# Kernel optimization log

Measured on AMD Instinct MI355X. Metric: run time of the kernel, lower is better.

The kernel has to match this reference:

```python
import jax, jax.numpy as jnp
import numpy as np

N = 50000   # nodes
E = 800000  # directed edges (built as reverse pairs so rev mapping is exact)
F = 64      # node_feat_dim
FE = 64     # edge_feat_dim
M = 64      # message_dim
S = 3       # num_status
L = 4       # number_layers

def _lin(key, din, dout):
    w = jax.random.normal(key, (din, dout), jnp.float32) * np.float32(1.0 / np.sqrt(din))
    return w, jnp.zeros((dout,), jnp.float32)

def setup_inputs() -> dict:
    key = jax.random.key(0)
    ks = jax.random.split(key, 16)
    half = E // 2
    s = jax.random.randint(ks[0], (half,), 0, N)
    t = jax.random.randint(ks[1], (half,), 0, N)
    src = jnp.concatenate([s, t])                      # source node of each edge
    tgt = jnp.concatenate([t, s])                      # target node of each edge
    rev = jnp.concatenate([jnp.arange(half, E), jnp.arange(half)])  # reverse-edge index
    inp = dict(src=src, tgt=tgt, rev=rev)
    inp['edge_feat_raw'] = jax.random.uniform(ks[2], (E, 1), jnp.float32)
    inp['node_prob'] = jax.random.uniform(ks[3], (N, 1), jnp.float32)
    inp['node_seed'] = (jax.random.uniform(ks[4], (N, 1)) < 0.05).astype(jnp.float32)
    inp['W_node'], inp['b_node'] = _lin(ks[5], 2, F)
    inp['W_edge'], inp['b_edge'] = _lin(ks[6], 1, FE)
    inp['W_init'], inp['b_init'] = _lin(ks[7], F + FE, M)
    inp['W_aggr'], inp['b_aggr'] = _lin(ks[8], M, M)
    inp['W_out'], inp['b_out'] = _lin(ks[9], M + F, S)
    inp['W_me'], inp['b_me'] = _lin(ks[10], FE + M, M)
    inp['W_mp'], inp['b_mp'] = _lin(ks[11], M, M)
    inp['W_ih'] = jax.random.normal(ks[12], (3 * M, M), jnp.float32) * np.float32(1.0 / np.sqrt(M))
    inp['W_hh'] = jax.random.normal(ks[13], (3 * M, M), jnp.float32) * np.float32(1.0 / np.sqrt(M))
    inp['b_ih'] = jnp.zeros((3 * M,), jnp.float32)
    inp['b_hh'] = jnp.zeros((3 * M,), jnp.float32)
    return inp

def reference(src, tgt, rev, edge_feat_raw, node_prob, node_seed,
              W_node, b_node, W_edge, b_edge, W_init, b_init,
              W_aggr, b_aggr, W_out, b_out, W_me, b_me, W_mp, b_mp,
              W_ih, W_hh, b_ih, b_hh):
    relu = jax.nn.relu
    node_feat = relu(jnp.concatenate([node_prob, node_seed], 1) @ W_node + b_node)  # [N,F]
    snode_feat = node_feat[src]                                                      # snode2edge gather [E,F]
    edge_feat = relu(edge_feat_raw @ W_edge + b_edge)                                # [E,FE]
    message = relu(jnp.concatenate([snode_feat, edge_feat], 1) @ W_init + b_init)    # [E,M]

    def nodes_out(msg):
        agg = jax.ops.segment_sum(msg, tgt, num_segments=N)                          # edge2tnode scatter-add
        agg = relu(agg @ W_aggr + b_aggr)
        logits = relu(jnp.concatenate([agg, node_feat], 1) @ W_out + b_out)
        return jax.nn.log_softmax(logits, axis=1)                                    # [N,S]

    def gru(x, h):  # torch.nn.GRUCell semantics
        gi = x @ W_ih.T + b_ih
        gh = h @ W_hh.T + b_hh
        ir, iz, in_ = jnp.split(gi, 3, axis=1)
        hr, hz, hn = jnp.split(gh, 3, axis=1)
        r = jax.nn.sigmoid(ir + hr)
        z = jax.nn.sigmoid(iz + hz)
        n = jnp.tanh(in_ + r * hn)
        return (1.0 - z) * n + z * h

    marg = [nodes_out(message)]
    deltas = []
    for _ in range(L):
        m = relu(jnp.concatenate([message, edge_feat], 1) @ W_me + b_me)
        node_agg = jax.ops.segment_sum(m, tgt, num_segments=N)
        m = node_agg[src] - m[rev]                                                   # nb_matrix (non-backtracking) spmm
        m = relu(m @ W_mp + b_mp)
        message = gru(m, message)
        marg.append(nodes_out(message))
        deltas.append(jnp.max(jnp.abs(jnp.exp(marg[-2][:, -1]) - jnp.exp(marg[-1][:, -1]))))
    return jnp.stack(marg, 0), jnp.stack(deltas)
```

## Files before the change

### kernel.cpp

```cpp
#include <hip/hip_runtime.h>
#include <hip/hip_fp16.h>

typedef _Float16 half8 __attribute__((ext_vector_type(8)));
typedef float floatx4 __attribute__((ext_vector_type(4)));

#define DEV static __device__ __forceinline__

DEV float sigmoidf_(float x) { return 1.f / (1.f + __expf(-x)); }
DEV float tanh_fast(float x) {
    x = fminf(fmaxf(x, -15.f), 15.f);
    float e2 = __expf(2.f * x);
    return (e2 - 1.f) / (e2 + 1.f);
}
DEV unsigned short f2h_(float f) {
    __half h = __float2half_rn(f);
    return *reinterpret_cast<unsigned short*>(&h);
}
DEV float h2f_(unsigned short u) {
    __half h = *reinterpret_cast<__half*>(&u);
    return __half2float(h);
}
DEV float loadElem(const float* p) { return *p; }
DEV float loadElem(const unsigned short* p) { return h2f_(*p); }
DEV void storeMsg(float* p, float v) { *p = v; }
DEV void storeMsg(unsigned short* p, float v) { *p = f2h_(v); }

DEV half8 afrag(const float* __restrict__ p, int koff) {
    float4 a = *reinterpret_cast<const float4*>(p + koff);
    float4 b = *reinterpret_cast<const float4*>(p + koff + 4);
    half8 h;
    h[0] = (_Float16)a.x; h[1] = (_Float16)a.y; h[2] = (_Float16)a.z; h[3] = (_Float16)a.w;
    h[4] = (_Float16)b.x; h[5] = (_Float16)b.y; h[6] = (_Float16)b.z; h[7] = (_Float16)b.w;
    return h;
}
DEV half8 afrag(const unsigned short* __restrict__ p, int koff) {
    uint4 v = *reinterpret_cast<const uint4*>(p + koff);
    return __builtin_bit_cast(half8, v);
}
DEV half8 h8load(const _Float16* __restrict__ p) {
    return *reinterpret_cast<const half8*>(p);
}
DEV half8 effrag(float er, const float* __restrict__ We,
                 const float* __restrict__ be, int k0) {
    float4 w0 = *reinterpret_cast<const float4*>(We + k0);
    float4 w1 = *reinterpret_cast<const float4*>(We + k0 + 4);
    float4 b0 = *reinterpret_cast<const float4*>(be + k0);
    float4 b1 = *reinterpret_cast<const float4*>(be + k0 + 4);
    half8 h;
    h[0] = (_Float16)fmaxf(fmaf(er, w0.x, b0.x), 0.f);
    h[1] = (_Float16)fmaxf(fmaf(er, w0.y, b0.y), 0.f);
    h[2] = (_Float16)fmaxf(fmaf(er, w0.z, b0.z), 0.f);
    h[3] = (_Float16)fmaxf(fmaf(er, w0.w, b0.w), 0.f);
    h[4] = (_Float16)fmaxf(fmaf(er, w1.x, b1.x), 0.f);
    h[5] = (_Float16)fmaxf(fmaf(er, w1.y, b1.y), 0.f);
    h[6] = (_Float16)fmaxf(fmaf(er, w1.z, b1.z), 0.f);
    h[7] = (_Float16)fmaxf(fmaf(er, w1.w, b1.w), 0.f);
    return h;
}
DEV void load8(const float* __restrict__ p, float x[8]) {
    const float4* q = reinterpret_cast<const float4*>(p);
    float4 a = q[0], b = q[1];
    x[0] = a.x; x[1] = a.y; x[2] = a.z; x[3] = a.w;
    x[4] = b.x; x[5] = b.y; x[6] = b.z; x[7] = b.w;
}

__global__ void k_deg(const int* __restrict__ tgt, int* __restrict__ deg, int E) {
    int e = blockIdx.x * blockDim.x + threadIdx.x;
    if (e < E) atomicAdd(&deg[tgt[e]], 1);
}

__global__ __launch_bounds__(1024)
void k_scan(const int* __restrict__ deg, int* __restrict__ row_ptr,
            int* __restrict__ cursor, int N) {
    __shared__ int part[1024];
    int tid = threadIdx.x;
    int chunk = (N + 1023) / 1024;
    int lo = tid * chunk, hi = min(lo + chunk, N);
    int s = 0;
    for (int i = lo; i < hi; i++) s += deg[i];
    part[tid] = s;
    __syncthreads();
    for (int off = 1; off < 1024; off <<= 1) {
        int v = (tid >= off) ? part[tid - off] : 0;
        __syncthreads();
        part[tid] += v;
        __syncthreads();
    }
    int base = (tid == 0) ? 0 : part[tid - 1];
    for (int i = lo; i < hi; i++) {
        row_ptr[i] = base;
        cursor[i] = base;
        base += deg[i];
    }
    if (tid == 1023) row_ptr[N] = part[1023];
}

__global__ void k_fill(const int* __restrict__ tgt, int* __restrict__ cursor,
                       int* __restrict__ col_idx, int E) {
    int e = blockIdx.x * blockDim.x + threadIdx.x;
    if (e < E) {
        int pos = atomicAdd(&cursor[tgt[e]], 1);
        col_idx[pos] = e;
    }
}

__global__ void k_prep(const float* __restrict__ Wme, const float* __restrict__ Wmp,
                       const float* __restrict__ Wi, const float* __restrict__ Wih,
                       const float* __restrict__ Whh, _Float16* __restrict__ wp) {
    int t = blockIdx.x * blockDim.x + threadIdx.x;
    if (t < 8192) { int n = t >> 7, k = t & 127; wp[t] = (_Float16)Wme[k * 64 + n]; return; }
    int u = t - 8192;
    if (u < 4096) { int n = u >> 6, k = u & 63; wp[8192 + u] = (_Float16)Wmp[k * 64 + n]; return; }
    u -= 4096;
    if (u < 4096) { int n = u >> 6, k = u & 63; wp[12288 + u] = (_Float16)Wi[(64 + k) * 64 + n]; return; }
    u -= 4096;
    if (u < 12288) { wp[16384 + u] = (_Float16)Wih[u]; return; }
    u -= 12288;
    if (u < 12288) { wp[28672 + u] = (_Float16)Whh[u]; return; }
}

__global__ __launch_bounds__(256)
void k_zn(const float* __restrict__ prob, const float* __restrict__ seedp,
          const float* __restrict__ Wn, const float* __restrict__ bn,
          const float* __restrict__ Wi, const float* __restrict__ bi,
          float* __restrict__ zn, int N) {
    int n = blockIdx.x * blockDim.x + threadIdx.x;
    if (n >= N) return;
    float p = prob[n], sd = seedp[n];
    float acc[64];
#pragma unroll
    for (int j = 0; j < 64; j++) acc[j] = bi[j];
#pragma unroll 1
    for (int k = 0; k < 64; k++) {
        float nf = fmaxf(fmaf(p, Wn[k], fmaf(sd, Wn[64 + k], bn[k])), 0.f);
        const float* w = Wi + k * 64;
#pragma unroll
        for (int j = 0; j < 64; j++) acc[j] = fmaf(nf, w[j], acc[j]);
    }
    float4* q = reinterpret_cast<float4*>(zn + (size_t)n * 64);
#pragma unroll
    for (int c = 0; c < 16; c++)
        q[c] = make_float4(acc[4 * c], acc[4 * c + 1], acc[4 * c + 2], acc[4 * c + 3]);
}

template <typename MsgT>
__global__ __launch_bounds__(256)
void k_init_mfma(const int* __restrict__ src, const float* __restrict__ eraw,
                 const float* __restrict__ We, const float* __restrict__ be,
                 const _Float16* __restrict__ WibT, const float* __restrict__ zn,
                 MsgT* __restrict__ message, int E) {
    int wid = (blockIdx.x * blockDim.x + threadIdx.x) >> 6;
    int rowbase = wid * 64;
    if (rowbase >= E) return;
    int lane = threadIdx.x & 63, q = lane >> 4, m16 = lane & 15, kq8 = q * 8;
    floatx4 zero4 = {0.f, 0.f, 0.f, 0.f};
    floatx4 acc[4][4];
#pragma unroll
    for (int a = 0; a < 4; a++)
#pragma unroll
        for (int b = 0; b < 4; b++) acc[a][b] = zero4;
#pragma unroll
    for (int ks = 0; ks < 2; ks++) {
        int k0 = ks * 32 + kq8;
        half8 B[4];
#pragma unroll
        for (int nt = 0; nt < 4; nt++) B[nt] = h8load(WibT + (nt * 16 + m16) * 64 + k0);
#pragma unroll
        for (int rt = 0; rt < 4; rt++) {
            int row = min(rowbase + rt * 16 + m16, E - 1);
            half8 A = effrag(eraw[row], We, be, k0);
#pragma unroll
            for (int nt = 0; nt < 4; nt++)
                acc[rt][nt] = __builtin_amdgcn_mfma_f32_16x16x32_f16(A, B[nt], acc[rt][nt], 0, 0, 0);
        }
    }
#pragma unroll
    for (int nt = 0; nt < 4; nt++) {
        int col = nt * 16 + m16;
#pragma unroll
        for (int rt = 0; rt < 4; rt++)
#pragma unroll
            for (int r = 0; r < 4; r++) {
                int row = rowbase + rt * 16 + q * 4 + r;
                if (row < E) {
                    int s = src[row];
                    float v = acc[rt][nt][r] + zn[(size_t)s * 64 + col];
                    storeMsg(message + (size_t)row * 64 + col, fmaxf(v, 0.f));
                }
            }
    }
}

template <typename MsgT>
__global__ __launch_bounds__(256)
void k_edge_m_mfma(const float* __restrict__ eraw, const float* __restrict__ We,
                   const float* __restrict__ be, const _Float16* __restrict__ WmeT,
                   const float* __restrict__ bme, const MsgT* __restrict__ message,
                   unsigned short* __restrict__ m_buf, int E) {
    int wid = (blockIdx.x * blockDim.x + threadIdx.x) >> 6;
    int rowbase = wid * 64;
    if (rowbase >= E) return;
    int lane = threadIdx.x & 63, q = lane >> 4, m16 = lane & 15, kq8 = q * 8;
    floatx4 zero4 = {0.f, 0.f, 0.f, 0.f};
    floatx4 acc[4][4];
#pragma unroll
    for (int a = 0; a < 4; a++)
#pragma unroll
        for (int b = 0; b < 4; b++) acc[a][b] = zero4;
#pragma unroll
    for (int ks = 0; ks < 4; ks++) {
        int k0 = ks * 32 + kq8;
        half8 B[4];
#pragma unroll
        for (int nt = 0; nt < 4; nt++) B[nt] = h8load(WmeT + (nt * 16 + m16) * 128 + k0);
#pragma unroll
        for (int rt = 0; rt < 4; rt++) {
            int row = min(rowbase + rt * 16 + m16, E - 1);
            half8 A = (ks < 2) ? afrag(message + (size_t)row * 64, k0)
                               : effrag(eraw[row], We, be, k0 - 64);
#pragma unroll
            for (int nt = 0; nt < 4; nt++)
                acc[rt][nt] = __builtin_amdgcn_mfma_f32_16x16x32_f16(A, B[nt], acc[rt][nt], 0, 0, 0);
        }
    }
#pragma unroll
    for (int nt = 0; nt < 4; nt++) {
        int col = nt * 16 + m16;
        float bb = bme[col];
#pragma unroll
        for (int rt = 0; rt < 4; rt++)
#pragma unroll
            for (int r = 0; r < 4; r++) {
                int row = rowbase + rt * 16 + q * 4 + r;
                if (row < E)
                    m_buf[(size_t)row * 64 + col] = f2h_(fmaxf(acc[rt][nt][r] + bb, 0.f));
            }
    }
}

template <typename MsgT>
__global__ __launch_bounds__(256)
void k_gru_mfma(const int* __restrict__ src, const int* __restrict__ rev,
                const float* __restrict__ node_agg,
                const unsigned short* __restrict__ m_buf,
                const _Float16* __restrict__ WmpT, const float* __restrict__ bmp,
                const _Float16* __restrict__ WihP, const _Float16* __restrict__ WhhP,
                const float* __restrict__ bih, const float* __restrict__ bhh,
                MsgT* __restrict__ message, int E) {
    __shared__ _Float16 uT[4][64 * 72];
    int wid = (blockIdx.x * blockDim.x + threadIdx.x) >> 6;
    int rowbase = wid * 64;
    if (rowbase >= E) return;
    int w = threadIdx.x >> 6;
    int lane = threadIdx.x & 63, q = lane >> 4, m16 = lane & 15, kq8 = q * 8;
    floatx4 zero4 = {0.f, 0.f, 0.f, 0.f};

    floatx4 accU[4][4];
#pragma unroll
    for (int a = 0; a < 4; a++)
#pragma unroll
        for (int b = 0; b < 4; b++) accU[a][b] = zero4;
#pragma unroll
    for (int ks = 0; ks < 2; ks++) {
        int k0 = ks * 32 + kq8;
        half8 B[4];
#pragma unroll
        for (int nt = 0; nt < 4; nt++) B[nt] = h8load(WmpT + (nt * 16 + m16) * 64 + k0);
#pragma unroll
        for (int rt = 0; rt < 4; rt++) {
            int row = min(rowbase + rt * 16 + m16, E - 1);
            int s = src[row], rv = rev[row];
            const float* na = node_agg + (size_t)s * 64 + k0;
            float4 a0 = *reinterpret_cast<const float4*>(na);
            float4 a1 = *reinterpret_cast<const float4*>(na + 4);
            uint4 mv = *reinterpret_cast<const uint4*>(m_buf + (size_t)rv * 64 + k0);
            half8 mh = __builtin_bit_cast(half8, mv);
            half8 A;
            A[0] = (_Float16)(a0.x - (float)mh[0]); A[1] = (_Float16)(a0.y - (float)mh[1]);
            A[2] = (_Float16)(a0.z - (float)mh[2]); A[3] = (_Float16)(a0.w - (float)mh[3]);
            A[4] = (_Float16)(a1.x - (float)mh[4]); A[5] = (_Float16)(a1.y - (float)mh[5]);
            A[6] = (_Float16)(a1.z - (float)mh[6]); A[7] = (_Float16)(a1.w - (float)mh[7]);
#pragma unroll
            for (int nt = 0; nt < 4; nt++)
                accU[rt][nt] = __builtin_amdgcn_mfma_f32_16x16x32_f16(A, B[nt], accU[rt][nt], 0, 0, 0);
        }
    }
#pragma unroll
    for (int nt = 0; nt < 4; nt++) {
        int col = nt * 16 + m16;
        float bb = bmp[col];
#pragma unroll
        for (int rt = 0; rt < 4; rt++)
#pragma unroll
            for (int r = 0; r < 4; r++) {
                int rl = rt * 16 + q * 4 + r;
                uT[w][rl * 72 + col] = (_Float16)fmaxf(accU[rt][nt][r] + bb, 0.f);
            }
    }
    half8 au[4][2], ah[4][2];
#pragma unroll
    for (int rt = 0; rt < 4; rt++)
#pragma unroll
        for (int ks = 0; ks < 2; ks++) {
            au[rt][ks] = *reinterpret_cast<const half8*>(
                &uT[w][(rt * 16 + m16) * 72 + ks * 32 + kq8]);
            int row = min(rowbase + rt * 16 + m16, E - 1);
            ah[rt][ks] = afrag(message + (size_t)row * 64, ks * 32 + kq8);
        }
#pragma unroll 1
    for (int nt = 0; nt < 4; nt++) {
        int col = nt * 16 + m16;
        half8 Bir[2], Biz[2], Bin[2], Bhr[2], Bhz[2], Bhn[2];
#pragma unroll
        for (int ks = 0; ks < 2; ks++) {
            int k0 = ks * 32 + kq8;
            Bir[ks] = h8load(WihP + (size_t)(0 + col) * 64 + k0);
            Biz[ks] = h8load(WihP + (size_t)(64 + col) * 64 + k0);
            Bin[ks] = h8load(WihP + (size_t)(128 + col) * 64 + k0);
            Bhr[ks] = h8load(WhhP + (size_t)(0 + col) * 64 + k0);
            Bhz[ks] = h8load(WhhP + (size_t)(64 + col) * 64 + k0);
            Bhn[ks] = h8load(WhhP + (size_t)(128 + col) * 64 + k0);
        }
        floatx4 ar[4], az[4], ain[4], ahn[4];
#pragma unroll
        for (int rt = 0; rt < 4; rt++) { ar[rt] = zero4; az[rt] = zero4; ain[rt] = zero4; ahn[rt] = zero4; }
#pragma unroll
        for (int ks = 0; ks < 2; ks++)
#pragma unroll
            for (int rt = 0; rt < 4; rt++) {
                ar[rt] = __builtin_amdgcn_mfma_f32_16x16x32_f16(au[rt][ks], Bir[ks], ar[rt], 0, 0, 0);
                ar[rt] = __builtin_amdgcn_mfma_f32_16x16x32_f16(ah[rt][ks], Bhr[ks], ar[rt], 0, 0, 0);
                az[rt] = __builtin_amdgcn_mfma_f32_16x16x32_f16(au[rt][ks], Biz[ks], az[rt], 0, 0, 0);
                az[rt] = __builtin_amdgcn_mfma_f32_16x16x32_f16(ah[rt][ks], Bhz[ks], az[rt], 0, 0, 0);
                ain[rt] = __builtin_amdgcn_mfma_f32_16x16x32_f16(au[rt][ks], Bin[ks], ain[rt], 0, 0, 0);
                ahn[rt] = __builtin_amdgcn_mfma_f32_16x16x32_f16(ah[rt][ks], Bhn[ks], ahn[rt], 0, 0, 0);
            }
        float br_ = bih[col] + bhh[col];
        float bz_ = bih[64 + col] + bhh[64 + col];
        float bin_ = bih[128 + col];
        float bhn_ = bhh[128 + col];
#pragma unroll
        for (int rt = 0; rt < 4; rt++)
#pragma unroll
            for (int r = 0; r < 4; r++) {
                int row = rowbase + rt * 16 + q * 4 + r;
                if (row < E) {
                    float rr = sigmoidf_(ar[rt][r] + br_);
                    float zz = sigmoidf_(az[rt][r] + bz_);
                    float nn = tanh_fast(ain[rt][r] + bin_ + rr * (ahn[rt][r] + bhn_));
                    MsgT* mp = message + (size_t)row * 64 + col;
                    float hv = loadElem(mp);
                    storeMsg(mp, fmaf(zz, hv - nn, nn));
                }
            }
    }
}

template <typename T>
__global__ __launch_bounds__(256)
void k_agg(const int* __restrict__ row_ptr, const int* __restrict__ col_idx,
           const T* __restrict__ rows, float* __restrict__ out, int N) {
    int wid = (blockIdx.x * blockDim.x + threadIdx.x) >> 6;
    int lane = threadIdx.x & 63;
    if (wid >= N) return;
    int beg = row_ptr[wid], end = row_ptr[wid + 1];
    float acc = 0.f;
    int i = beg;
    for (; i + 1 < end; i += 2) {
        int e0 = __builtin_amdgcn_readfirstlane(col_idx[i]);
        int e1 = __builtin_amdgcn_readfirstlane(col_idx[i + 1]);
        acc += loadElem(rows + (size_t)e0 * 64 + lane);
        acc += loadElem(rows + (size_t)e1 * 64 + lane);
    }
    if (i < end) {
        int e0 = __builtin_amdgcn_readfirstlane(col_idx[i]);
        acc += loadElem(rows + (size_t)e0 * 64 + lane);
    }
    out[(size_t)wid * 64 + lane] = acc;
}

__global__ __launch_bounds__(256, 2)
void k_nodes(const float* __restrict__ node_agg, const float* __restrict__ prob,
             const float* __restrict__ seedp,
             const float* __restrict__ Wn, const float* __restrict__ bn,
             const float* __restrict__ Wa, const float* __restrict__ ba,
             const float* __restrict__ Wo, const float* __restrict__ bo,
             float* __restrict__ marg, float* __restrict__ prev_p2,
             float* __restrict__ deltas_f, int layer, int N) {
    int n = blockIdx.x * blockDim.x + threadIdx.x;
    if (n >= N) return;
    float a[64];
#pragma unroll
    for (int j = 0; j < 64; j++) a[j] = ba[j];
    const float* ag = node_agg + (size_t)n * 64;
#pragma unroll 1
    for (int c = 0; c < 8; c++) {
        float v[8];
        load8(ag + 8 * c, v);
#pragma unroll
        for (int i = 0; i < 8; i++) {
            const float* w = Wa + (8 * c + i) * 64;
#pragma unroll
            for (int j = 0; j < 64; j++) a[j] = fmaf(v[i], w[j], a[j]);
        }
    }
    float l0 = bo[0], l1 = bo[1], l2 = bo[2];
#pragma unroll
    for (int k = 0; k < 64; k++) {
        float ak = fmaxf(a[k], 0.f);
        l0 = fmaf(ak, Wo[k * 3 + 0], l0);
        l1 = fmaf(ak, Wo[k * 3 + 1], l1);
        l2 = fmaf(ak, Wo[k * 3 + 2], l2);
    }
    float p = prob[n], sd = seedp[n];
#pragma unroll 1
    for (int k = 0; k < 64; k++) {
        float nf = fmaxf(fmaf(p, Wn[k], fmaf(sd, Wn[64 + k], bn[k])), 0.f);
        l0 = fmaf(nf, Wo[(64 + k) * 3 + 0], l0);
        l1 = fmaf(nf, Wo[(64 + k) * 3 + 1], l1);
        l2 = fmaf(nf, Wo[(64 + k) * 3 + 2], l2);
    }
    l0 = fmaxf(l0, 0.f); l1 = fmaxf(l1, 0.f); l2 = fmaxf(l2, 0.f);
    float mx = fmaxf(l0, fmaxf(l1, l2));
    float ssum = __expf(l0 - mx) + __expf(l1 - mx) + __expf(l2 - mx);
    float lse = mx + logf(ssum);
    float o0 = l0 - lse, o1 = l1 - lse, o2 = l2 - lse;
    float* out = marg + ((size_t)layer * N + n) * 3;
    out[0] = o0; out[1] = o1; out[2] = o2;
    float p2 = __expf(o2);
    if (layer > 0) {
        float d = fabsf(p2 - prev_p2[n]);
        atomicMax(reinterpret_cast<unsigned int*>(deltas_f + (layer - 1)),
                  __float_as_uint(d));
    }
    prev_p2[n] = p2;
}

__global__ void k_deltas_out(const float* __restrict__ deltas_f,
                             float* __restrict__ out, int L) {
    int i = threadIdx.x;
    if (i < L) out[i] = deltas_f[i];
}

template <typename MsgT>
static void run_pipeline(void* const* d_in, int E, int N, MsgT* message,
                         unsigned short* m_buf, float* node_agg, _Float16* wp,
                         int* deg, int* row_ptr, int* cursor, int* col_idx,
                         float* prev_p2, float* deltas_f, float* marg,
                         float* deltas_out, hipStream_t stream) {
    const int* src = (const int*)d_in[0];
    const int* tgt = (const int*)d_in[1];
    const int* rev = (const int*)d_in[2];
    const float* eraw = (const float*)d_in[3];
    const float* prob = (const float*)d_in[4];
    const float* seedp = (const float*)d_in[5];
    const float* Wn = (const float*)d_in[6];  const float* bn = (const float*)d_in[7];
    const float* We = (const float*)d_in[8];  const float* be = (const float*)d_in[9];
    const float* Wi = (const float*)d_in[10]; const float* bi = (const float*)d_in[11];
    const float* Wa = (const float*)d_in[12]; const float* ba = (const float*)d_in[13];
    const float* Wo = (const float*)d_in[14]; const float* bo = (const float*)d_in[15];
    const float* Wme = (const float*)d_in[16]; const float* bme = (const float*)d_in[17];
    const float* Wmp = (const float*)d_in[18]; const float* bmp = (const float*)d_in[19];
    const float* Wih = (const float*)d_in[20]; const float* Whh = (const float*)d_in[21];
    const float* bih = (const float*)d_in[22]; const float* bhh = (const float*)d_in[23];

    const _Float16* WmeT = wp;
    const _Float16* WmpT = wp + 8192;
    const _Float16* WibT = wp + 12288;
    const _Float16* WihP = wp + 16384;
    const _Float16* WhhP = wp + 28672;

    const int L = 4;
    dim3 blk(256);
    dim3 eg((E + 255) / 256), ng((N + 255) / 256);
    dim3 ag((N + 3) / 4);
    int waves = (E + 63) / 64;
    dim3 mg((waves + 3) / 4);

    hipMemsetAsync(deg, 0, (size_t)N * 4, stream);
    hipMemsetAsync(deltas_f, 0, L * sizeof(float), stream);
    k_deg<<<eg, blk, 0, stream>>>(tgt, deg, E);
    k_scan<<<1, 1024, 0, stream>>>(deg, row_ptr, cursor, N);
    k_fill<<<eg, blk, 0, stream>>>(tgt, cursor, col_idx, E);
    k_prep<<<160, 256, 0, stream>>>(Wme, Wmp, Wi, Wih, Whh, wp);
    k_zn<<<ng, blk, 0, stream>>>(prob, seedp, Wn, bn, Wi, bi, node_agg, N);
    k_init_mfma<MsgT><<<mg, blk, 0, stream>>>(src, eraw, We, be, WibT,
                                              node_agg, message, E);
    k_agg<MsgT><<<ag, blk, 0, stream>>>(row_ptr, col_idx, message, node_agg, N);
    k_nodes<<<ng, blk, 0, stream>>>(node_agg, prob, seedp, Wn, bn, Wa, ba, Wo, bo,
                                    marg, prev_p2, deltas_f, 0, N);
    for (int l = 0; l < L; l++) {
        k_edge_m_mfma<MsgT><<<mg, blk, 0, stream>>>(eraw, We, be, WmeT, bme,
                                                    message, m_buf, E);
        k_agg<unsigned short><<<ag, blk, 0, stream>>>(row_ptr, col_idx, m_buf,
                                                      node_agg, N);
        k_gru_mfma<MsgT><<<mg, blk, 0, stream>>>(src, rev, node_agg, m_buf,
                                                 WmpT, bmp, WihP, WhhP, bih, bhh,
                                                 message, E);
        k_agg<MsgT><<<ag, blk, 0, stream>>>(row_ptr, col_idx, message, node_agg, N);
        k_nodes<<<ng, blk, 0, stream>>>(node_agg, prob, seedp, Wn, bn, Wa, ba,
                                        Wo, bo, marg, prev_p2, deltas_f, l + 1, N);
    }
    k_deltas_out<<<1, 64, 0, stream>>>(deltas_f, deltas_out, L);
}

extern "C" void kernel_launch(void* const* d_in, const int* in_sizes, int n_in,
                              void* d_out, int out_size, void* d_ws, size_t ws_size,
                              hipStream_t stream) {
    const int E = in_sizes[0];
    const int N = in_sizes[4];
    const int L = 4, S = 3;

    float* marg = (float*)d_out;
    float* deltas_out = marg + (size_t)(L + 1) * N * S;

    char* ws = (char*)d_ws;
    float* deltas_f = (float*)ws;
    float* prev_p2 = (float*)(ws + 16);
    int* deg = (int*)(prev_p2 + N);
    int* row_ptr = deg + N;
    int* cursor = row_ptr + N + 1;
    int* col_idx = cursor + N;
    char* p = (char*)(col_idx + E);
    p = (char*)(((uintptr_t)p + 255) & ~(uintptr_t)255);
    _Float16* wp = (_Float16*)p;
    p += 40960 * 2;
    p = (char*)(((uintptr_t)p + 255) & ~(uintptr_t)255);
    float* node_agg = (float*)p;
    p += (size_t)N * 64 * 4;
    p = (char*)(((uintptr_t)p + 255) & ~(uintptr_t)255);
    size_t head = (size_t)(p - ws);
    size_t msg_f32 = (size_t)E * 64 * 4;
    size_t msg_f16 = (size_t)E * 64 * 2;
    size_t m_f16 = (size_t)E * 64 * 2;

    if (ws_size >= head + msg_f32 + m_f16) {
        float* message = (float*)p;
        unsigned short* m_buf = (unsigned short*)(p + msg_f32);
        run_pipeline<float>(d_in, E, N, message, m_buf, node_agg, wp,
                            deg, row_ptr, cursor, col_idx,
                            prev_p2, deltas_f, marg, deltas_out, stream);
    } else {
        unsigned short* message = (unsigned short*)p;
        unsigned short* m_buf = (unsigned short*)(p + msg_f16);
        run_pipeline<unsigned short>(d_in, E, N, message, m_buf, node_agg, wp,
                                     deg, row_ptr, cursor, col_idx,
                                     prev_p2, deltas_f, marg, deltas_out, stream);
    }
}
```

Baseline: 2.469 ms.

## Split edge kernels into full/tail launches, use 32-bit indexing, extract h via MFMA

The edge MFMA kernels are templated on a FULL flag. Full 256-row blocks skip row clamping and bounds checks, and a single separate launch handles the tail. Address arithmetic moves from size_t to unsigned 32-bit to save 64-bit integer ops. The GRU kernel recovers the previous hidden value from the already loaded A fragments with an identity-matrix MFMA instead of reloading it from global memory. The CSR aggregation loop is unrolled by four. Together these cut instruction count and memory traffic, at the cost of an extra tail launch and an overflow risk if E*64 exceeds 32 bits.

```diff
diff --git a/kernel.cpp b/kernel.cpp
--- a/kernel.cpp
+++ b/kernel.cpp
@@ -25,16 +25,16 @@
 DEV void storeMsg(float* p, float v) { *p = v; }
 DEV void storeMsg(unsigned short* p, float v) { *p = f2h_(v); }
 
-DEV half8 afrag(const float* __restrict__ p, int koff) {
-    float4 a = *reinterpret_cast<const float4*>(p + koff);
-    float4 b = *reinterpret_cast<const float4*>(p + koff + 4);
+DEV half8 afrag(const float* __restrict__ p, unsigned off) {
+    float4 a = *reinterpret_cast<const float4*>(p + off);
+    float4 b = *reinterpret_cast<const float4*>(p + off + 4);
     half8 h;
     h[0] = (_Float16)a.x; h[1] = (_Float16)a.y; h[2] = (_Float16)a.z; h[3] = (_Float16)a.w;
     h[4] = (_Float16)b.x; h[5] = (_Float16)b.y; h[6] = (_Float16)b.z; h[7] = (_Float16)b.w;
     return h;
 }
-DEV half8 afrag(const unsigned short* __restrict__ p, int koff) {
-    uint4 v = *reinterpret_cast<const uint4*>(p + koff);
+DEV half8 afrag(const unsigned short* __restrict__ p, unsigned off) {
+    uint4 v = *reinterpret_cast<const uint4*>(p + off);
     return __builtin_bit_cast(half8, v);
 }
 DEV half8 h8load(const _Float16* __restrict__ p) {
@@ -143,14 +143,14 @@
         q[c] = make_float4(acc[4 * c], acc[4 * c + 1], acc[4 * c + 2], acc[4 * c + 3]);
 }
 
-template <typename MsgT>
+template <typename MsgT, bool FULL>
 __global__ __launch_bounds__(256)
 void k_init_mfma(const int* __restrict__ src, const float* __restrict__ eraw,
                  const float* __restrict__ We, const float* __restrict__ be,
                  const _Float16* __restrict__ WibT, const float* __restrict__ zn,
-                 MsgT* __restrict__ message, int E) {
+                 MsgT* __restrict__ message, int row_off, int E) {
     int wid = (blockIdx.x * blockDim.x + threadIdx.x) >> 6;
-    int rowbase = wid * 64;
+    int rowbase = row_off + wid * 64;
     if (rowbase >= E) return;
     int lane = threadIdx.x & 63, q = lane >> 4, m16 = lane & 15, kq8 = q * 8;
     floatx4 zero4 = {0.f, 0.f, 0.f, 0.f};
@@ -167,7 +167,8 @@
         for (int nt = 0; nt < 4; nt++) B[nt] = h8load(WibT + (nt * 16 + m16) * 64 + k0);
 #pragma unroll
         for (int rt = 0; rt < 4; rt++) {
-            int row = min(rowbase + rt * 16 + m16, E - 1);
+            int row = rowbase + rt * 16 + m16;
+            if (!FULL) row = min(row, E - 1);
             half8 A = effrag(eraw[row], We, be, k0);
 #pragma unroll
             for (int nt = 0; nt < 4; nt++)
@@ -182,23 +183,23 @@
 #pragma unroll
             for (int r = 0; r < 4; r++) {
                 int row = rowbase + rt * 16 + q * 4 + r;
-                if (row < E) {
+                if (FULL || row < E) {
                     int s = src[row];
-                    float v = acc[rt][nt][r] + zn[(size_t)s * 64 + col];
-                    storeMsg(message + (size_t)row * 64 + col, fmaxf(v, 0.f));
+                    float v = acc[rt][nt][r] + zn[(unsigned)s * 64u + col];
+                    storeMsg(message + (unsigned)row * 64u + col, fmaxf(v, 0.f));
                 }
             }
     }
 }
 
-template <typename MsgT>
+template <typename MsgT, bool FULL>
 __global__ __launch_bounds__(256)
 void k_edge_m_mfma(const float* __restrict__ eraw, const float* __restrict__ We,
                    const float* __restrict__ be, const _Float16* __restrict__ WmeT,
                    const float* __restrict__ bme, const MsgT* __restrict__ message,
-                   unsigned short* __restrict__ m_buf, int E) {
+                   unsigned short* __restrict__ m_buf, int row_off, int E) {
     int wid = (blockIdx.x * blockDim.x + threadIdx.x) >> 6;
-    int rowbase = wid * 64;
+    int rowbase = row_off + wid * 64;
     if (rowbase >= E) return;
     int lane = threadIdx.x & 63, q = lane >> 4, m16 = lane & 15, kq8 = q * 8;
     floatx4 zero4 = {0.f, 0.f, 0.f, 0.f};
@@ -215,8 +216,9 @@
         for (int nt = 0; nt < 4; nt++) B[nt] = h8load(WmeT + (nt * 16 + m16) * 128 + k0);
 #pragma unroll
         for (int rt = 0; rt < 4; rt++) {
-            int row = min(rowbase + rt * 16 + m16, E - 1);
-            half8 A = (ks < 2) ? afrag(message + (size_t)row * 64, k0)
+            int row = rowbase + rt * 16 + m16;
+            if (!FULL) row = min(row, E - 1);
+            half8 A = (ks < 2) ? afrag(message + (unsigned)row * 64u, k0)
                                : effrag(eraw[row], We, be, k0 - 64);
 #pragma unroll
             for (int nt = 0; nt < 4; nt++)
@@ -232,13 +234,13 @@
 #pragma unroll
             for (int r = 0; r < 4; r++) {
                 int row = rowbase + rt * 16 + q * 4 + r;
-                if (row < E)
-                    m_buf[(size_t)row * 64 + col] = f2h_(fmaxf(acc[rt][nt][r] + bb, 0.f));
+                if (FULL || row < E)
+                    m_buf[(unsigned)row * 64u + col] = f2h_(fmaxf(acc[rt][nt][r] + bb, 0.f));
             }
     }
 }
 
-template <typename MsgT>
+template <typename MsgT, bool FULL>
 __global__ __launch_bounds__(256)
 void k_gru_mfma(const int* __restrict__ src, const int* __restrict__ rev,
                 const float* __restrict__ node_agg,
@@ -246,10 +248,10 @@
                 const _Float16* __restrict__ WmpT, const float* __restrict__ bmp,
                 const _Float16* __restrict__ WihP, const _Float16* __restrict__ WhhP,
                 const float* __restrict__ bih, const float* __restrict__ bhh,
-                MsgT* __restrict__ message, int E) {
+                MsgT* __restrict__ message, int row_off, int E) {
     __shared__ _Float16 uT[4][64 * 72];
     int wid = (blockIdx.x * blockDim.x + threadIdx.x) >> 6;
-    int rowbase = wid * 64;
+    int rowbase = row_off + wid * 64;
     if (rowbase >= E) return;
     int w = threadIdx.x >> 6;
     int lane = threadIdx.x & 63, q = lane >> 4, m16 = lane & 15, kq8 = q * 8;
@@ -268,12 +270,13 @@
         for (int nt = 0; nt < 4; nt++) B[nt] = h8load(WmpT + (nt * 16 + m16) * 64 + k0);
 #pragma unroll
         for (int rt = 0; rt < 4; rt++) {
-            int row = min(rowbase + rt * 16 + m16, E - 1);
+            int row = rowbase + rt * 16 + m16;
+            if (!FULL) row = min(row, E - 1);
             int s = src[row], rv = rev[row];
-            const float* na = node_agg + (size_t)s * 64 + k0;
+            const float* na = node_agg + (unsigned)s * 64u + k0;
             float4 a0 = *reinterpret_cast<const float4*>(na);
             float4 a1 = *reinterpret_cast<const float4*>(na + 4);
-            uint4 mv = *reinterpret_cast<const uint4*>(m_buf + (size_t)rv * 64 + k0);
+            uint4 mv = *reinterpret_cast<const uint4*>(m_buf + (unsigned)rv * 64u + k0);
             half8 mh = __builtin_bit_cast(half8, mv);
             half8 A;
             A[0] = (_Float16)(a0.x - (float)mh[0]); A[1] = (_Float16)(a0.y - (float)mh[1]);
@@ -304,8 +307,9 @@
         for (int ks = 0; ks < 2; ks++) {
             au[rt][ks] = *reinterpret_cast<const half8*>(
                 &uT[w][(rt * 16 + m16) * 72 + ks * 32 + kq8]);
-            int row = min(rowbase + rt * 16 + m16, E - 1);
-            ah[rt][ks] = afrag(message + (size_t)row * 64, ks * 32 + kq8);
+            int row = rowbase + rt * 16 + m16;
+            if (!FULL) row = min(row, E - 1);
+            ah[rt][ks] = afrag(message + (unsigned)row * 64u, ks * 32 + kq8);
         }
 #pragma unroll 1
     for (int nt = 0; nt < 4; nt++) {
@@ -314,16 +318,24 @@
 #pragma unroll
         for (int ks = 0; ks < 2; ks++) {
             int k0 = ks * 32 + kq8;
-            Bir[ks] = h8load(WihP + (size_t)(0 + col) * 64 + k0);
-            Biz[ks] = h8load(WihP + (size_t)(64 + col) * 64 + k0);
-            Bin[ks] = h8load(WihP + (size_t)(128 + col) * 64 + k0);
-            Bhr[ks] = h8load(WhhP + (size_t)(0 + col) * 64 + k0);
-            Bhz[ks] = h8load(WhhP + (size_t)(64 + col) * 64 + k0);
-            Bhn[ks] = h8load(WhhP + (size_t)(128 + col) * 64 + k0);
-        }
-        floatx4 ar[4], az[4], ain[4], ahn[4];
-#pragma unroll
-        for (int rt = 0; rt < 4; rt++) { ar[rt] = zero4; az[rt] = zero4; ain[rt] = zero4; ahn[rt] = zero4; }
+            Bir[ks] = h8load(WihP + (unsigned)(0 + col) * 64u + k0);
+            Biz[ks] = h8load(WihP + (unsigned)(64 + col) * 64u + k0);
+            Bin[ks] = h8load(WihP + (unsigned)(128 + col) * 64u + k0);
+            Bhr[ks] = h8load(WhhP + (unsigned)(0 + col) * 64u + k0);
+            Bhz[ks] = h8load(WhhP + (unsigned)(64 + col) * 64u + k0);
+            Bhn[ks] = h8load(WhhP + (unsigned)(128 + col) * 64u + k0);
+        }
+        int tgtk = (nt & 1) * 16 + m16;
+        half8 If;
+#pragma unroll
+        for (int j = 0; j < 8; j++) If[j] = (_Float16)((kq8 + j == tgtk) ? 1.f : 0.f);
+        int ksI = nt >> 1;
+        floatx4 ar[4], az[4], ain[4], ahn[4], Dh[4];
+#pragma unroll
+        for (int rt = 0; rt < 4; rt++) {
+            ar[rt] = zero4; az[rt] = zero4; ain[rt] = zero4; ahn[rt] = zero4;
+            Dh[rt] = __builtin_amdgcn_mfma_f32_16x16x32_f16(ah[rt][ksI], If, zero4, 0, 0, 0);
+        }
 #pragma unroll
         for (int ks = 0; ks < 2; ks++)
 #pragma unroll
@@ -344,13 +356,12 @@
 #pragma unroll
             for (int r = 0; r < 4; r++) {
                 int row = rowbase + rt * 16 + q * 4 + r;
-                if (row < E) {
+                if (FULL || row < E) {
                     float rr = sigmoidf_(ar[rt][r] + br_);
                     float zz = sigmoidf_(az[rt][r] + bz_);
                     float nn = tanh_fast(ain[rt][r] + bin_ + rr * (ahn[rt][r] + bhn_));
-                    MsgT* mp = message + (size_t)row * 64 + col;
-                    float hv = loadElem(mp);
-                    storeMsg(mp, fmaf(zz, hv - nn, nn));
+                    float hv = Dh[rt][r];
+                    storeMsg(message + (unsigned)row * 64u + col, fmaf(zz, hv - nn, nn));
                 }
             }
     }
@@ -366,17 +377,21 @@
     int beg = row_ptr[wid], end = row_ptr[wid + 1];
     float acc = 0.f;
     int i = beg;
-    for (; i + 1 < end; i += 2) {
+    for (; i + 3 < end; i += 4) {
         int e0 = __builtin_amdgcn_readfirstlane(col_idx[i]);
         int e1 = __builtin_amdgcn_readfirstlane(col_idx[i + 1]);
-        acc += loadElem(rows + (size_t)e0 * 64 + lane);
-        acc += loadElem(rows + (size_t)e1 * 64 + lane);
-    }
-    if (i < end) {
+        int e2 = __builtin_amdgcn_readfirstlane(col_idx[i + 2]);
+        int e3 = __builtin_amdgcn_readfirstlane(col_idx[i + 3]);
+        acc += loadElem(rows + (unsigned)e0 * 64u + lane);
+        acc += loadElem(rows + (unsigned)e1 * 64u + lane);
+        acc += loadElem(rows + (unsigned)e2 * 64u + lane);
+        acc += loadElem(rows + (unsigned)e3 * 64u + lane);
+    }
+    for (; i < end; i++) {
         int e0 = __builtin_amdgcn_readfirstlane(col_idx[i]);
-        acc += loadElem(rows + (size_t)e0 * 64 + lane);
-    }
-    out[(size_t)wid * 64 + lane] = acc;
+        acc += loadElem(rows + (unsigned)e0 * 64u + lane);
+    }
+    out[(unsigned)wid * 64u + lane] = acc;
 }
 
 __global__ __launch_bounds__(256, 2)
@@ -474,8 +489,9 @@
     dim3 blk(256);
     dim3 eg((E + 255) / 256), ng((N + 255) / 256);
     dim3 ag((N + 3) / 4);
-    int waves = (E + 63) / 64;
-    dim3 mg((waves + 3) / 4);
+    int fullb = E / 256;
+    int tail_off = fullb * 256;
+    bool tail = (tail_off < E);
 
     hipMemsetAsync(deg, 0, (size_t)N * 4, stream);
     hipMemsetAsync(deltas_f, 0, L * sizeof(float), stream);
@@ -484,19 +500,33 @@
     k_fill<<<eg, blk, 0, stream>>>(tgt, cursor, col_idx, E);
     k_prep<<<160, 256, 0, stream>>>(Wme, Wmp, Wi, Wih, Whh, wp);
     k_zn<<<ng, blk, 0, stream>>>(prob, seedp, Wn, bn, Wi, bi, node_agg, N);
-    k_init_mfma<MsgT><<<mg, blk, 0, stream>>>(src, eraw, We, be, WibT,
-                                              node_agg, message, E);
+
+    if (fullb)
+        k_init_mfma<MsgT, true><<<fullb, blk, 0, stream>>>(src, eraw, We, be, WibT,
+                                                           node_agg, message, 0, E);
+    if (tail)
+        k_init_mfma<MsgT, false><<<1, blk, 0, stream>>>(src, eraw, We, be, WibT,
+                                                        node_agg, message, tail_off, E);
     k_agg<MsgT><<<ag, blk, 0, stream>>>(row_ptr, col_idx, message, node_agg, N);
     k_nodes<<<ng, blk, 0, stream>>>(node_agg, prob, seedp, Wn, bn, Wa, ba, Wo, bo,
                                     marg, prev_p2, deltas_f, 0, N);
     for (int l = 0; l < L; l++) {
-        k_edge_m_mfma<MsgT><<<mg, blk, 0, stream>>>(eraw, We, be, WmeT, bme,
-                                                    message, m_buf, E);
+        if (fullb)
+            k_edge_m_mfma<MsgT, true><<<fullb, blk, 0, stream>>>(eraw, We, be, WmeT, bme,
+                                                                 message, m_buf, 0, E);
+        if (tail)
+            k_edge_m_mfma<MsgT, false><<<1, blk, 0, stream>>>(eraw, We, be, WmeT, bme,
+                                                              message, m_buf, tail_off, E);
         k_agg<unsigned short><<<ag, blk, 0, stream>>>(row_ptr, col_idx, m_buf,
                                                       node_agg, N);
-        k_gru_mfma<MsgT><<<mg, blk, 0, stream>>>(src, rev, node_agg, m_buf,
-                                                 WmpT, bmp, WihP, WhhP, bih, bhh,
-                                                 message, E);
+        if (fullb)
+            k_gru_mfma<MsgT, true><<<fullb, blk, 0, stream>>>(src, rev, node_agg, m_buf,
+                                                              WmpT, bmp, WihP, WhhP,
+                                                              bih, bhh, message, 0, E);
+        if (tail)
+            k_gru_mfma<MsgT, false><<<1, blk, 0, stream>>>(src, rev, node_agg, m_buf,
+                                                           WmpT, bmp, WihP, WhhP,
+                                                           bih, bhh, message, tail_off, E);
         k_agg<MsgT><<<ag, blk, 0, stream>>>(row_ptr, col_idx, message, node_agg, N);
         k_nodes<<<ng, blk, 0, stream>>>(node_agg, prob, seedp, Wn, bn, Wa, ba,
                                         Wo, bo, marg, prev_p2, deltas_f, l + 1, N);
```

Result: slower. 4.921 ms (+99.3%).
